# Kernel tuning notes

Hardware: AMD Instinct MI355X
Metric: run time of the kernel (lower is better)

## Reference

```python
import jax, jax.numpy as jnp
import numpy as np

D, N, F_IN, F_OUT = 2, 4096, 128, 128
DENSITY = 0.005  # avg degree ~20 per row in the 0/1 attention graphs
NEG_INF = -1e30


def setup_inputs() -> dict:
    key = jax.random.key(0)
    ks = jax.random.split(key, 12)
    X = jax.random.normal(ks[0], (D, N, F_IN), dtype=jnp.float32)
    # Dense Laplacian operator used in torch.sparse.mm(L[i], h_p); scaled so tanh stays non-degenerate
    L = jax.random.normal(ks[1], (D, N, N), dtype=jnp.float32) / np.float32(np.sqrt(N))
    # Upper/lower adjacency: 0/1 matrices (GATLayer extracts edges via adj == 1)
    L_u = (jax.random.uniform(ks[2], (D, N, N)) < DENSITY).astype(jnp.float32)
    L_d = (jax.random.uniform(ks[3], (D, N, N)) < DENSITY).astype(jnp.float32)
    s = np.float32(0.05)
    Wp = jax.random.normal(ks[4], (D, F_IN, F_OUT), dtype=jnp.float32) * s
    Ws = jax.random.normal(ks[5], (D, F_IN, F_OUT), dtype=jnp.float32) * s
    Wu = jax.random.normal(ks[6], (D, F_IN, F_OUT), dtype=jnp.float32) * s
    au1 = jax.random.normal(ks[7], (D, F_OUT), dtype=jnp.float32) * s
    au2 = jax.random.normal(ks[8], (D, F_OUT), dtype=jnp.float32) * s
    Wd = jax.random.normal(ks[9], (D, F_IN, F_OUT), dtype=jnp.float32) * s
    ad1 = jax.random.normal(ks[10], (D, F_OUT), dtype=jnp.float32) * s
    ad2 = jax.random.normal(ks[11], (D, F_OUT), dtype=jnp.float32) * s
    return {"X": X, "L": L, "L_u": L_u, "L_d": L_d,
            "Wp": Wp, "Ws": Ws, "Wu": Wu, "au1": au1, "au2": au2,
            "Wd": Wd, "ad1": ad1, "ad2": ad2, "dimensions": D}


def _gat(x, adj, W, a1, a2):
    # GATLayer.forward with boundary=False: linear -> edge scores -> LeakyReLU ->
    # row-wise softmax restricted to adj==1 entries -> sparse mm.
    h = x @ W                                   # [N, F_OUT]
    s1 = h @ a1                                 # [N]  (a_1 linear, bias=False)
    s2 = h @ a2                                 # [N]
    scores = jax.nn.leaky_relu(s1[:, None] + s2[None, :])  # [N, N], slope 0.01
    mask = adj == 1.0
    scores = jnp.where(mask, scores, NEG_INF)
    attn = jax.nn.softmax(scores, axis=1)
    attn = jnp.where(mask, attn, 0.0)           # zero rows with no edges (sparse softmax semantics)
    return attn @ h                             # [N, F_OUT]


def _san_dim(x, L, Lu, Ld, Wp, Ws, Wu, au1, au2, Wd, ad1, ad2):
    h_p = jnp.tanh(L @ (x @ Wp))
    h_s = jnp.tanh(x @ Ws)
    h_u = jnp.tanh(_gat(x, Lu, Wu, au1, au2))
    h_d = jnp.tanh(_gat(x, Ld, Wd, ad1, ad2))
    return h_s + h_u + h_d + h_p


def reference(X, L, L_u, L_d, Wp, Ws, Wu, au1, au2, Wd, ad1, ad2, dimensions):
    # vmap over the `dimensions` simplex levels (all per-level params stacked on axis 0)
    return jax.vmap(_san_dim)(X, L, L_u, L_d, Wp, Ws, Wu, au1, au2, Wd, ad1, ad2)
```

## Files before the change

### kernel.cpp

```cpp
#include <hip/hip_runtime.h>
#include <hip/hip_bf16.h>

#define NN 4096
#define FD 128
#define NDIM 2
#define CAP 256

typedef unsigned long long u64;

#define OFF_HMAT 0
#define OFF_SVEC 3145728
#define OFF_HP   3178496
#define OFF_GU   7372800
#define OFF_GD   8421376
#define OFF_H0T  9469952
#define OFF_MASK 9994240

typedef _Float16 f16x8 __attribute__((ext_vector_type(8)));
typedef float f32x4 __attribute__((ext_vector_type(4)));
typedef float f32x4v __attribute__((ext_vector_type(4)));
typedef unsigned long long u64x2 __attribute__((ext_vector_type(2)));

union P4 { _Float16 h[4]; int2 i2; };

__device__ __forceinline__ float f4get(const float4& v, int j) {
    return j == 0 ? v.x : j == 1 ? v.y : j == 2 ? v.z : v.w;
}

__global__ __launch_bounds__(256) void k_xw(
    const float* __restrict__ X, const float* __restrict__ Wp,
    const float* __restrict__ Wsm, const float* __restrict__ Wu,
    const float* __restrict__ Wd, float* __restrict__ hmat,
    _Float16* __restrict__ h0T) {
  int d = blockIdx.z, p = blockIdx.y;
  int r0 = blockIdx.x * 128;
  const float* W = (p == 0 ? Wp : p == 1 ? Wsm : p == 2 ? Wu : Wd) + (size_t)d * FD * FD;
  const float* Xd = X + ((size_t)d * NN + r0) * FD;
  __shared__ int4 As4[2048];
  __shared__ int4 Bs4[2048];
  char* As = (char*)As4; char* Bs = (char*)Bs4;
  int t = threadIdx.x;

#pragma unroll 4
  for (int u = 0; u < 16; u++) {
    int id = t + u * 256;
    int row = id >> 5, k4 = (id & 31) * 4;
    float4 v = *(const float4*)(Xd + (size_t)row * FD + k4);
    P4 pk;
    pk.h[0] = (_Float16)v.x; pk.h[1] = (_Float16)v.y;
    pk.h[2] = (_Float16)v.z; pk.h[3] = (_Float16)v.w;
    int off = (row * 256 + k4 * 2) ^ ((row & 7) << 4);
    *(int2*)(As + off) = pk.i2;
  }
#pragma unroll 4
  for (int u = 0; u < 16; u++) {
    int id = t + u * 256;
    int k = id >> 5, n4 = (id & 31) * 4;
    float4 v = *(const float4*)(W + (size_t)k * FD + n4);
#pragma unroll
    for (int j = 0; j < 4; j++) {
      int n = n4 + j;
      int off = (n * 256 + k * 2) ^ ((n & 7) << 4);
      *(_Float16*)(Bs + off) = (_Float16)f4get(v, j);
    }
  }
  __syncthreads();

  int w = t >> 6, l = t & 63;
  int lr = l & 15, lkb = (l >> 4) * 16;
  f32x4 acc[2][8] = {};
#pragma unroll
  for (int kb = 0; kb < 4; kb++) {
    f16x8 a[2], b[8];
#pragma unroll
    for (int m = 0; m < 2; m++) {
      int row = w * 32 + m * 16 + lr;
      int off = (row * 256 + kb * 64 + lkb) ^ ((row & 7) << 4);
      a[m] = *(const f16x8*)(As + off);
    }
#pragma unroll
    for (int n = 0; n < 8; n++) {
      int rn = n * 16 + lr;
      int off = (rn * 256 + kb * 64 + lkb) ^ ((rn & 7) << 4);
      b[n] = *(const f16x8*)(Bs + off);
    }
#pragma unroll
    for (int m = 0; m < 2; m++)
#pragma unroll
      for (int n = 0; n < 8; n++)
        acc[m][n] = __builtin_amdgcn_mfma_f32_16x16x32_f16(a[m], b[n], acc[m][n], 0, 0, 0);
  }

  if (p == 0) {
    _Float16* hT = h0T + (size_t)d * FD * NN;
#pragma unroll
    for (int m = 0; m < 2; m++)
#pragma unroll
      for (int n = 0; n < 8; n++) {
        int col = n * 16 + lr;
        int grow = r0 + w * 32 + m * 16 + (l >> 4) * 4;
        P4 pk;
#pragma unroll
        for (int r = 0; r < 4; r++) pk.h[r] = (_Float16)acc[m][n][r];
        *(int2*)(hT + (size_t)col * NN + grow) = pk.i2;
      }
  } else {
    float* o = hmat + ((size_t)(d * 3 + p - 1) * NN + r0) * FD;
#pragma unroll
    for (int m = 0; m < 2; m++)
#pragma unroll
      for (int n = 0; n < 8; n++)
#pragma unroll
        for (int r = 0; r < 4; r++)
          o[(size_t)(w * 32 + m * 16 + (l >> 4) * 4 + r) * FD + n * 16 + lr] = acc[m][n][r];
  }
}

__global__ __launch_bounds__(256) void k_svec(
    const float* __restrict__ hmat, const float* __restrict__ au1,
    const float* __restrict__ au2, const float* __restrict__ ad1,
    const float* __restrict__ ad2, float* __restrict__ svec) {
  int v = blockIdx.y, d = blockIdx.z;
  int w = threadIdx.x >> 6, lane = threadIdx.x & 63;
  int i = blockIdx.x * 4 + w;
  const float* a = (v == 0 ? au1 : v == 1 ? au2 : v == 2 ? ad1 : ad2) + (size_t)d * FD;
  const float* h = hmat + ((size_t)(d * 3 + 1 + (v >> 1)) * NN + i) * FD;
  float x = h[lane] * a[lane] + h[64 + lane] * a[64 + lane];
#pragma unroll
  for (int o = 1; o < 64; o <<= 1) x += __shfl_xor(x, o);
  if (lane == 0) svec[(size_t)(d * 4 + v) * NN + i] = x;
}

__global__ __launch_bounds__(256) void k_lgemm(
    const float* __restrict__ L, const _Float16* __restrict__ h0T,
    float* __restrict__ hp) {
  int d = blockIdx.z, ks = blockIdx.y;
  int r0 = blockIdx.x * 64;
  const float* Lr = L + (size_t)d * NN * NN;
  const _Float16* hT = h0T + (size_t)d * FD * NN;
  __shared__ int4 As4[512];
  __shared__ int4 Bs4[1024];
  char* As = (char*)As4; char* Bs = (char*)Bs4;
  int t = threadIdx.x;
  int w = t >> 6, l = t & 63;
  int lr = l & 15, lkb = (l >> 4) * 16;
  f32x4 acc[8] = {};
  int kbeg = ks * 1024;
  for (int kk = kbeg; kk < kbeg + 1024; kk += 64) {
#pragma unroll
    for (int u = 0; u < 4; u++) {
      int id = t + u * 256;
      int row = id >> 4, k4 = (id & 15) * 4;
      f32x4v v = __builtin_nontemporal_load(
          (const f32x4v*)(Lr + (size_t)(r0 + row) * NN + kk) + (k4 >> 2));
      P4 pk;
      pk.h[0] = (_Float16)v[0]; pk.h[1] = (_Float16)v[1];
      pk.h[2] = (_Float16)v[2]; pk.h[3] = (_Float16)v[3];
      int off = (row * 128 + k4 * 2) ^ ((row & 7) << 4);
      *(int2*)(As + off) = pk.i2;
    }
#pragma unroll
    for (int u = 0; u < 4; u++) {
      int id = t + u * 256;
      int n = id >> 3, k8 = (id & 7) * 8;
      int4 v = *(const int4*)(hT + (size_t)n * NN + kk + k8);
      int off = (n * 128 + k8 * 2) ^ ((n & 7) << 4);
      *(int4*)(Bs + off) = v;
    }
    __syncthreads();
#pragma unroll
    for (int kb = 0; kb < 2; kb++) {
      int row = w * 16 + lr;
      int offA = (row * 128 + kb * 64 + lkb) ^ ((row & 7) << 4);
      f16x8 a = *(const f16x8*)(As + offA);
      f16x8 b[8];
#pragma unroll
      for (int n = 0; n < 8; n++) {
        int rn = n * 16 + lr;
        int off = (rn * 128 + kb * 64 + lkb) ^ ((rn & 7) << 4);
        b[n] = *(const f16x8*)(Bs + off);
      }
#pragma unroll
      for (int n = 0; n < 8; n++)
        acc[n] = __builtin_amdgcn_mfma_f32_16x16x32_f16(a, b[n], acc[n], 0, 0, 0);
    }
    __syncthreads();
  }
  float* o = hp + ((size_t)(d * 4 + ks) * NN + r0) * FD;
#pragma unroll
  for (int n = 0; n < 8; n++)
#pragma unroll
    for (int r = 0; r < 4; r++)
      o[(size_t)(w * 16 + (l >> 4) * 4 + r) * FD + n * 16 + lr] = acc[n][r];
}

__global__ __launch_bounds__(256) void k_pack(
    const float* __restrict__ Lu, const float* __restrict__ Ldn,
    u64* __restrict__ mask) {
  int lane = threadIdx.x & 63;
  int wid = (blockIdx.x * 256 + threadIdx.x) >> 6;
  int nw = (gridDim.x * 256) >> 6;
  const int QTOT = 4 * NN * 2;
  for (int quad = wid; quad < QTOT; quad += nw) {
    int p = quad >> 13;
    int rq = quad & 8191;
    int row = rq >> 1, half = rq & 1;
    const float* src = ((p & 1) ? Ldn : Lu) +
                       ((size_t)(p >> 1) * NN + row) * (size_t)NN + half * 2048;
    f32x4v v[8];
#pragma unroll
    for (int q = 0; q < 4; q++) {
      const f32x4v* s4 = (const f32x4v*)(src + q * 512);
      v[2 * q]     = __builtin_nontemporal_load(s4 + lane);
      v[2 * q + 1] = __builtin_nontemporal_load(s4 + 64 + lane);
    }
    u64* o = mask + ((size_t)p * NN + row) * 64 + half * 32;
#pragma unroll
    for (int q = 0; q < 4; q++) {
      u64 m0 = __ballot(v[2 * q][0] == 1.0f);
      u64 m1 = __ballot(v[2 * q][1] == 1.0f);
      u64 m2 = __ballot(v[2 * q][2] == 1.0f);
      u64 m3 = __ballot(v[2 * q][3] == 1.0f);
      u64 m4 = __ballot(v[2 * q + 1][0] == 1.0f);
      u64 m5 = __ballot(v[2 * q + 1][1] == 1.0f);
      u64 m6 = __ballot(v[2 * q + 1][2] == 1.0f);
      u64 m7 = __ballot(v[2 * q + 1][3] == 1.0f);
      if (lane == 0) {
        u64x2 a0 = {m0, m1}, a1 = {m2, m3}, a2 = {m4, m5}, a3 = {m6, m7};
        __builtin_nontemporal_store(a0, (u64x2*)(o + q * 8 + 0));
        __builtin_nontemporal_store(a1, (u64x2*)(o + q * 8 + 2));
        __builtin_nontemporal_store(a2, (u64x2*)(o + q * 8 + 4));
        __builtin_nontemporal_store(a3, (u64x2*)(o + q * 8 + 6));
      }
    }
  }
}

__global__ __launch_bounds__(256) void k_gat2(
    const u64* __restrict__ mask, const float* __restrict__ hmat,
    const float* __restrict__ svec, float* __restrict__ gu,
    float* __restrict__ gd) {
  int d = blockIdx.z, a = blockIdx.y;
  int w = threadIdx.x >> 6, lane = threadIdx.x & 63;
  int i = blockIdx.x * 4 + w;
  const u64* mrow = mask + ((size_t)((d * 2 + a) * NN) + i) * 64;
  const float* h = hmat + (size_t)(d * 3 + 1 + a) * NN * FD;
  const float* s1 = svec + (size_t)(d * 4 + 2 * a) * NN;
  const float* s2 = svec + (size_t)(d * 4 + 2 * a + 1) * NN;
  float* g = (a ? gd : gu) + ((size_t)d * NN + i) * FD;

  __shared__ int ej[4][CAP];
  __shared__ float wt[4][CAP];

  u64 m = mrow[lane];
  int c = __popcll(m);
  int pre = c;
#pragma unroll
  for (int o = 1; o < 64; o <<= 1) {
    int tv = __shfl_up(pre, o);
    if (lane >= o) pre += tv;
  }
  int cnt = __shfl(pre, 63);
  int base = pre - c;
  int colbase = (lane >> 2) * 256 + (lane & 3);
  while (m) {
    int b = __ffsll((unsigned long long)m) - 1;
    m &= m - 1;
    if (base < CAP) ej[w][base] = colbase + b * 4;
    base++;
  }
  cnt = min(cnt, CAP);

  float s1i = s1[i];
  float mx = -1e30f;
  for (int e0 = 0; e0 < cnt; e0 += 64) {
    int e = e0 + lane;
    float sc = -1e30f;
    if (e < cnt) {
      int j = ej[w][e];
      float x = s1i + s2[j];
      sc = x > 0.0f ? x : 0.01f * x;
      wt[w][e] = sc;
    }
    mx = fmaxf(mx, sc);
  }
#pragma unroll
  for (int o = 1; o < 64; o <<= 1) mx = fmaxf(mx, __shfl_xor(mx, o));
  float sum = 0.0f;
  for (int e0 = 0; e0 < cnt; e0 += 64) {
    int e = e0 + lane;
    float pv = 0.0f;
    if (e < cnt) {
      pv = expf(wt[w][e] - mx);
      wt[w][e] = pv;
    }
    sum += pv;
  }
#pragma unroll
  for (int o = 1; o < 64; o <<= 1) sum += __shfl_xor(sum, o);
  float inv = (cnt > 0) ? 1.0f / sum : 0.0f;

  float acc0 = 0.0f, acc1 = 0.0f;
  int e = 0;
  for (; e + 4 <= cnt; e += 4) {
    const float* r0 = h + (size_t)ej[w][e + 0] * FD;
    const float* r1 = h + (size_t)ej[w][e + 1] * FD;
    const float* r2 = h + (size_t)ej[w][e + 2] * FD;
    const float* r3 = h + (size_t)ej[w][e + 3] * FD;
    float w0 = wt[w][e + 0] * inv, w1 = wt[w][e + 1] * inv;
    float w2 = wt[w][e + 2] * inv, w3 = wt[w][e + 3] * inv;
    float a0 = r0[lane], b0 = r0[64 + lane];
    float a1 = r1[lane], b1 = r1[64 + lane];
    float a2 = r2[lane], b2 = r2[64 + lane];
    float a3 = r3[lane], b3 = r3[64 + lane];
    acc0 += w0 * a0 + w1 * a1 + w2 * a2 + w3 * a3;
    acc1 += w0 * b0 + w1 * b1 + w2 * b2 + w3 * b3;
  }
  for (; e < cnt; e++) {
    float wg = wt[w][e] * inv;
    const float* hr = h + (size_t)ej[w][e] * FD;
    acc0 += wg * hr[lane];
    acc1 += wg * hr[64 + lane];
  }
  g[lane] = acc0;
  g[64 + lane] = acc1;
}

__global__ __launch_bounds__(256) void k_combine(
    const float* __restrict__ hmat, const float* __restrict__ hp,
    const float* __restrict__ gu, const float* __restrict__ gd,
    float* __restrict__ out) {
  const size_t tot4 = (size_t)NDIM * NN * FD / 4;
  for (size_t i4 = (size_t)blockIdx.x * blockDim.x + threadIdx.x; i4 < tot4;
       i4 += (size_t)gridDim.x * blockDim.x) {
    size_t i = i4 * 4;
    int d = (int)(i >> 19);
    size_t rem = i & 524287;
    float4 hs = *(const float4*)(hmat + ((size_t)(d * 3) << 19) + rem);
    float4 p0 = *(const float4*)(hp + ((size_t)(d * 4 + 0) << 19) + rem);
    float4 p1 = *(const float4*)(hp + ((size_t)(d * 4 + 1) << 19) + rem);
    float4 p2 = *(const float4*)(hp + ((size_t)(d * 4 + 2) << 19) + rem);
    float4 p3 = *(const float4*)(hp + ((size_t)(d * 4 + 3) << 19) + rem);
    float4 u = *(const float4*)(gu + ((size_t)d << 19) + rem);
    float4 dd = *(const float4*)(gd + ((size_t)d << 19) + rem);
    float4 o;
    o.x = tanhf(hs.x) + tanhf(u.x) + tanhf(dd.x) + tanhf(p0.x + p1.x + p2.x + p3.x);
    o.y = tanhf(hs.y) + tanhf(u.y) + tanhf(dd.y) + tanhf(p0.y + p1.y + p2.y + p3.y);
    o.z = tanhf(hs.z) + tanhf(u.z) + tanhf(dd.z) + tanhf(p0.z + p1.z + p2.z + p3.z);
    o.w = tanhf(hs.w) + tanhf(u.w) + tanhf(dd.w) + tanhf(p0.w + p1.w + p2.w + p3.w);
    *(float4*)(out + i) = o;
  }
}

extern "C" void kernel_launch(void* const* d_in, const int* in_sizes, int n_in,
                              void* d_out, int out_size, void* d_ws, size_t ws_size,
                              hipStream_t stream) {
  const float* X   = (const float*)d_in[0];
  const float* L   = (const float*)d_in[1];
  const float* Lu  = (const float*)d_in[2];
  const float* Ldn = (const float*)d_in[3];
  const float* Wp  = (const float*)d_in[4];
  const float* Wsm = (const float*)d_in[5];
  const float* Wu  = (const float*)d_in[6];
  const float* au1 = (const float*)d_in[7];
  const float* au2 = (const float*)d_in[8];
  const float* Wd  = (const float*)d_in[9];
  const float* ad1 = (const float*)d_in[10];
  const float* ad2 = (const float*)d_in[11];
  float* out = (float*)d_out;
  float* ws = (float*)d_ws;

  float* hmat = ws + OFF_HMAT;
  float* svec = ws + OFF_SVEC;
  float* hp   = ws + OFF_HP;
  float* gu   = ws + OFF_GU;
  float* gd   = ws + OFF_GD;
  _Float16* h0T = (_Float16*)(ws + OFF_H0T);
  u64* mask = (u64*)(ws + OFF_MASK);

  k_xw<<<dim3(NN / 128, 4, NDIM), 256, 0, stream>>>(X, Wp, Wsm, Wu, Wd, hmat, h0T);
  k_svec<<<dim3(NN / 4, 4, NDIM), 256, 0, stream>>>(hmat, au1, au2, ad1, ad2, svec);
  k_pack<<<2048, 256, 0, stream>>>(Lu, Ldn, mask);
  k_lgemm<<<dim3(NN / 64, 4, NDIM), 256, 0, stream>>>(L, h0T, hp);
  k_gat2<<<dim3(NN / 4, 2, NDIM), 256, 0, stream>>>(mask, hmat, svec, gu, gd);
  k_combine<<<1024, 256, 0, stream>>>(hmat, hp, gu, gd, out);
}
```

Baseline: 133.5 us.

## Merge L-GEMM with mask packing, fuse GAT with final combine

Runs the dense L GEMM and the adjacency bit-packing in one launch, using disjoint block ranges, so the compute-heavy and bandwidth-heavy work can share the GPU at the same time. The two GAT aggregations are fused with the tanh combine into one kernel, which removes the gu/gd intermediate buffers and their extra read/write pass. The fused GAT kernel uses twice the shared memory per block, which may reduce occupancy. It also does both attention passes serially within each wave.

```diff
diff --git a/kernel.cpp b/kernel.cpp
--- a/kernel.cpp
+++ b/kernel.cpp
@@ -11,10 +11,8 @@
 #define OFF_HMAT 0
 #define OFF_SVEC 3145728
 #define OFF_HP   3178496
-#define OFF_GU   7372800
-#define OFF_GD   8421376
-#define OFF_H0T  9469952
-#define OFF_MASK 9994240
+#define OFF_H0T  7372800
+#define OFF_MASK 7897088
 
 typedef _Float16 f16x8 __attribute__((ext_vector_type(8)));
 typedef float f32x4 __attribute__((ext_vector_type(4)));
@@ -131,224 +129,211 @@
   if (lane == 0) svec[(size_t)(d * 4 + v) * NN + i] = x;
 }
 
-__global__ __launch_bounds__(256) void k_lgemm(
+__global__ __launch_bounds__(256) void k_mega(
     const float* __restrict__ L, const _Float16* __restrict__ h0T,
-    float* __restrict__ hp) {
-  int d = blockIdx.z, ks = blockIdx.y;
-  int r0 = blockIdx.x * 64;
-  const float* Lr = L + (size_t)d * NN * NN;
-  const _Float16* hT = h0T + (size_t)d * FD * NN;
-  __shared__ int4 As4[512];
-  __shared__ int4 Bs4[1024];
-  char* As = (char*)As4; char* Bs = (char*)Bs4;
-  int t = threadIdx.x;
-  int w = t >> 6, l = t & 63;
-  int lr = l & 15, lkb = (l >> 4) * 16;
-  f32x4 acc[8] = {};
-  int kbeg = ks * 1024;
-  for (int kk = kbeg; kk < kbeg + 1024; kk += 64) {
-#pragma unroll
-    for (int u = 0; u < 4; u++) {
-      int id = t + u * 256;
-      int row = id >> 4, k4 = (id & 15) * 4;
-      f32x4v v = __builtin_nontemporal_load(
-          (const f32x4v*)(Lr + (size_t)(r0 + row) * NN + kk) + (k4 >> 2));
-      P4 pk;
-      pk.h[0] = (_Float16)v[0]; pk.h[1] = (_Float16)v[1];
-      pk.h[2] = (_Float16)v[2]; pk.h[3] = (_Float16)v[3];
-      int off = (row * 128 + k4 * 2) ^ ((row & 7) << 4);
-      *(int2*)(As + off) = pk.i2;
-    }
-#pragma unroll
-    for (int u = 0; u < 4; u++) {
-      int id = t + u * 256;
-      int n = id >> 3, k8 = (id & 7) * 8;
-      int4 v = *(const int4*)(hT + (size_t)n * NN + kk + k8);
-      int off = (n * 128 + k8 * 2) ^ ((n & 7) << 4);
-      *(int4*)(Bs + off) = v;
-    }
-    __syncthreads();
-#pragma unroll
-    for (int kb = 0; kb < 2; kb++) {
-      int row = w * 16 + lr;
-      int offA = (row * 128 + kb * 64 + lkb) ^ ((row & 7) << 4);
-      f16x8 a = *(const f16x8*)(As + offA);
-      f16x8 b[8];
-#pragma unroll
-      for (int n = 0; n < 8; n++) {
-        int rn = n * 16 + lr;
-        int off = (rn * 128 + kb * 64 + lkb) ^ ((rn & 7) << 4);
-        b[n] = *(const f16x8*)(Bs + off);
-      }
-#pragma unroll
-      for (int n = 0; n < 8; n++)
-        acc[n] = __builtin_amdgcn_mfma_f32_16x16x32_f16(a, b[n], acc[n], 0, 0, 0);
-    }
-    __syncthreads();
-  }
-  float* o = hp + ((size_t)(d * 4 + ks) * NN + r0) * FD;
-#pragma unroll
-  for (int n = 0; n < 8; n++)
-#pragma unroll
-    for (int r = 0; r < 4; r++)
-      o[(size_t)(w * 16 + (l >> 4) * 4 + r) * FD + n * 16 + lr] = acc[n][r];
-}
-
-__global__ __launch_bounds__(256) void k_pack(
+    float* __restrict__ hp,
     const float* __restrict__ Lu, const float* __restrict__ Ldn,
     u64* __restrict__ mask) {
-  int lane = threadIdx.x & 63;
-  int wid = (blockIdx.x * 256 + threadIdx.x) >> 6;
-  int nw = (gridDim.x * 256) >> 6;
-  const int QTOT = 4 * NN * 2;
-  for (int quad = wid; quad < QTOT; quad += nw) {
-    int p = quad >> 13;
-    int rq = quad & 8191;
-    int row = rq >> 1, half = rq & 1;
-    const float* src = ((p & 1) ? Ldn : Lu) +
-                       ((size_t)(p >> 1) * NN + row) * (size_t)NN + half * 2048;
-    f32x4v v[8];
-#pragma unroll
-    for (int q = 0; q < 4; q++) {
-      const f32x4v* s4 = (const f32x4v*)(src + q * 512);
-      v[2 * q]     = __builtin_nontemporal_load(s4 + lane);
-      v[2 * q + 1] = __builtin_nontemporal_load(s4 + 64 + lane);
-    }
-    u64* o = mask + ((size_t)p * NN + row) * 64 + half * 32;
-#pragma unroll
-    for (int q = 0; q < 4; q++) {
-      u64 m0 = __ballot(v[2 * q][0] == 1.0f);
-      u64 m1 = __ballot(v[2 * q][1] == 1.0f);
-      u64 m2 = __ballot(v[2 * q][2] == 1.0f);
-      u64 m3 = __ballot(v[2 * q][3] == 1.0f);
-      u64 m4 = __ballot(v[2 * q + 1][0] == 1.0f);
-      u64 m5 = __ballot(v[2 * q + 1][1] == 1.0f);
-      u64 m6 = __ballot(v[2 * q + 1][2] == 1.0f);
-      u64 m7 = __ballot(v[2 * q + 1][3] == 1.0f);
-      if (lane == 0) {
-        u64x2 a0 = {m0, m1}, a1 = {m2, m3}, a2 = {m4, m5}, a3 = {m6, m7};
-        __builtin_nontemporal_store(a0, (u64x2*)(o + q * 8 + 0));
-        __builtin_nontemporal_store(a1, (u64x2*)(o + q * 8 + 2));
-        __builtin_nontemporal_store(a2, (u64x2*)(o + q * 8 + 4));
-        __builtin_nontemporal_store(a3, (u64x2*)(o + q * 8 + 6));
-      }
-    }
-  }
-}
-
-__global__ __launch_bounds__(256) void k_gat2(
+  __shared__ int4 sm4[1536];
+  int t = threadIdx.x, w = t >> 6, lane = t & 63;
+
+  if (blockIdx.x < 512) {
+    int b = blockIdx.x;
+    int r0 = (b & 63) * 64, ks = (b >> 6) & 3, d = b >> 8;
+    const float* Lr = L + (size_t)d * NN * NN;
+    const _Float16* hT = h0T + (size_t)d * FD * NN;
+    char* As = (char*)sm4;
+    char* Bs = (char*)(sm4 + 512);
+    int lr = lane & 15, lkb = (lane >> 4) * 16;
+    f32x4 acc[8] = {};
+    int kbeg = ks * 1024;
+    for (int kk = kbeg; kk < kbeg + 1024; kk += 64) {
+#pragma unroll
+      for (int u = 0; u < 4; u++) {
+        int id = t + u * 256;
+        int row = id >> 4, k4 = (id & 15) * 4;
+        f32x4v v = __builtin_nontemporal_load(
+            (const f32x4v*)(Lr + (size_t)(r0 + row) * NN + kk) + (k4 >> 2));
+        P4 pk;
+        pk.h[0] = (_Float16)v[0]; pk.h[1] = (_Float16)v[1];
+        pk.h[2] = (_Float16)v[2]; pk.h[3] = (_Float16)v[3];
+        int off = (row * 128 + k4 * 2) ^ ((row & 7) << 4);
+        *(int2*)(As + off) = pk.i2;
+      }
+#pragma unroll
+      for (int u = 0; u < 4; u++) {
+        int id = t + u * 256;
+        int n = id >> 3, k8 = (id & 7) * 8;
+        int4 v = *(const int4*)(hT + (size_t)n * NN + kk + k8);
+        int off = (n * 128 + k8 * 2) ^ ((n & 7) << 4);
+        *(int4*)(Bs + off) = v;
+      }
+      __syncthreads();
+#pragma unroll
+      for (int kb = 0; kb < 2; kb++) {
+        int row = w * 16 + lr;
+        int offA = (row * 128 + kb * 64 + lkb) ^ ((row & 7) << 4);
+        f16x8 a = *(const f16x8*)(As + offA);
+        f16x8 bb[8];
+#pragma unroll
+        for (int n = 0; n < 8; n++) {
+          int rn = n * 16 + lr;
+          int off = (rn * 128 + kb * 64 + lkb) ^ ((rn & 7) << 4);
+          bb[n] = *(const f16x8*)(Bs + off);
+        }
+#pragma unroll
+        for (int n = 0; n < 8; n++)
+          acc[n] = __builtin_amdgcn_mfma_f32_16x16x32_f16(a, bb[n], acc[n], 0, 0, 0);
+      }
+      __syncthreads();
+    }
+    float* o = hp + ((size_t)(d * 4 + ks) * NN + r0) * FD;
+#pragma unroll
+    for (int n = 0; n < 8; n++)
+#pragma unroll
+      for (int r = 0; r < 4; r++)
+        o[(size_t)(w * 16 + (lane >> 4) * 4 + r) * FD + n * 16 + lr] = acc[n][r];
+    return;
+  }
+
+  int hr = (blockIdx.x - 512) * 4 + w;
+  int p = hr >> 13;
+  int rq = hr & 8191;
+  int row = rq >> 1, half = rq & 1;
+  const float* src = ((p & 1) ? Ldn : Lu) +
+                     ((size_t)(p >> 1) * NN + row) * (size_t)NN + half * 2048;
+  f32x4v v[8];
+#pragma unroll
+  for (int q = 0; q < 4; q++) {
+    const f32x4v* s4 = (const f32x4v*)(src + q * 512);
+    v[2 * q]     = __builtin_nontemporal_load(s4 + lane);
+    v[2 * q + 1] = __builtin_nontemporal_load(s4 + 64 + lane);
+  }
+  u64* o = mask + ((size_t)p * NN + row) * 64 + half * 32;
+#pragma unroll
+  for (int q = 0; q < 4; q++) {
+    u64 m0 = __ballot(v[2 * q][0] == 1.0f);
+    u64 m1 = __ballot(v[2 * q][1] == 1.0f);
+    u64 m2 = __ballot(v[2 * q][2] == 1.0f);
+    u64 m3 = __ballot(v[2 * q][3] == 1.0f);
+    u64 m4 = __ballot(v[2 * q + 1][0] == 1.0f);
+    u64 m5 = __ballot(v[2 * q + 1][1] == 1.0f);
+    u64 m6 = __ballot(v[2 * q + 1][2] == 1.0f);
+    u64 m7 = __ballot(v[2 * q + 1][3] == 1.0f);
+    if (lane == 0) {
+      u64x2 a0 = {m0, m1}, a1 = {m2, m3}, a2 = {m4, m5}, a3 = {m6, m7};
+      __builtin_nontemporal_store(a0, (u64x2*)(o + q * 8 + 0));
+      __builtin_nontemporal_store(a1, (u64x2*)(o + q * 8 + 2));
+      __builtin_nontemporal_store(a2, (u64x2*)(o + q * 8 + 4));
+      __builtin_nontemporal_store(a3, (u64x2*)(o + q * 8 + 6));
+    }
+  }
+}
+
+__global__ __launch_bounds__(256) void k_gatc(
     const u64* __restrict__ mask, const float* __restrict__ hmat,
-    const float* __restrict__ svec, float* __restrict__ gu,
-    float* __restrict__ gd) {
-  int d = blockIdx.z, a = blockIdx.y;
+    const float* __restrict__ svec, const float* __restrict__ hp,
+    float* __restrict__ out) {
+  int d = blockIdx.y;
   int w = threadIdx.x >> 6, lane = threadIdx.x & 63;
   int i = blockIdx.x * 4 + w;
-  const u64* mrow = mask + ((size_t)((d * 2 + a) * NN) + i) * 64;
-  const float* h = hmat + (size_t)(d * 3 + 1 + a) * NN * FD;
-  const float* s1 = svec + (size_t)(d * 4 + 2 * a) * NN;
-  const float* s2 = svec + (size_t)(d * 4 + 2 * a + 1) * NN;
-  float* g = (a ? gd : gu) + ((size_t)d * NN + i) * FD;
-
-  __shared__ int ej[4][CAP];
-  __shared__ float wt[4][CAP];
-
-  u64 m = mrow[lane];
-  int c = __popcll(m);
-  int pre = c;
-#pragma unroll
-  for (int o = 1; o < 64; o <<= 1) {
-    int tv = __shfl_up(pre, o);
-    if (lane >= o) pre += tv;
-  }
-  int cnt = __shfl(pre, 63);
-  int base = pre - c;
-  int colbase = (lane >> 2) * 256 + (lane & 3);
-  while (m) {
-    int b = __ffsll((unsigned long long)m) - 1;
-    m &= m - 1;
-    if (base < CAP) ej[w][base] = colbase + b * 4;
-    base++;
-  }
-  cnt = min(cnt, CAP);
-
-  float s1i = s1[i];
-  float mx = -1e30f;
-  for (int e0 = 0; e0 < cnt; e0 += 64) {
-    int e = e0 + lane;
-    float sc = -1e30f;
-    if (e < cnt) {
-      int j = ej[w][e];
-      float x = s1i + s2[j];
-      sc = x > 0.0f ? x : 0.01f * x;
-      wt[w][e] = sc;
-    }
-    mx = fmaxf(mx, sc);
-  }
-#pragma unroll
-  for (int o = 1; o < 64; o <<= 1) mx = fmaxf(mx, __shfl_xor(mx, o));
-  float sum = 0.0f;
-  for (int e0 = 0; e0 < cnt; e0 += 64) {
-    int e = e0 + lane;
-    float pv = 0.0f;
-    if (e < cnt) {
-      pv = expf(wt[w][e] - mx);
-      wt[w][e] = pv;
-    }
-    sum += pv;
-  }
-#pragma unroll
-  for (int o = 1; o < 64; o <<= 1) sum += __shfl_xor(sum, o);
-  float inv = (cnt > 0) ? 1.0f / sum : 0.0f;
-
-  float acc0 = 0.0f, acc1 = 0.0f;
-  int e = 0;
-  for (; e + 4 <= cnt; e += 4) {
-    const float* r0 = h + (size_t)ej[w][e + 0] * FD;
-    const float* r1 = h + (size_t)ej[w][e + 1] * FD;
-    const float* r2 = h + (size_t)ej[w][e + 2] * FD;
-    const float* r3 = h + (size_t)ej[w][e + 3] * FD;
-    float w0 = wt[w][e + 0] * inv, w1 = wt[w][e + 1] * inv;
-    float w2 = wt[w][e + 2] * inv, w3 = wt[w][e + 3] * inv;
-    float a0 = r0[lane], b0 = r0[64 + lane];
-    float a1 = r1[lane], b1 = r1[64 + lane];
-    float a2 = r2[lane], b2 = r2[64 + lane];
-    float a3 = r3[lane], b3 = r3[64 + lane];
-    acc0 += w0 * a0 + w1 * a1 + w2 * a2 + w3 * a3;
-    acc1 += w0 * b0 + w1 * b1 + w2 * b2 + w3 * b3;
-  }
-  for (; e < cnt; e++) {
-    float wg = wt[w][e] * inv;
-    const float* hr = h + (size_t)ej[w][e] * FD;
-    acc0 += wg * hr[lane];
-    acc1 += wg * hr[64 + lane];
-  }
-  g[lane] = acc0;
-  g[64 + lane] = acc1;
-}
-
-__global__ __launch_bounds__(256) void k_combine(
-    const float* __restrict__ hmat, const float* __restrict__ hp,
-    const float* __restrict__ gu, const float* __restrict__ gd,
-    float* __restrict__ out) {
-  const size_t tot4 = (size_t)NDIM * NN * FD / 4;
-  for (size_t i4 = (size_t)blockIdx.x * blockDim.x + threadIdx.x; i4 < tot4;
-       i4 += (size_t)gridDim.x * blockDim.x) {
-    size_t i = i4 * 4;
-    int d = (int)(i >> 19);
-    size_t rem = i & 524287;
-    float4 hs = *(const float4*)(hmat + ((size_t)(d * 3) << 19) + rem);
-    float4 p0 = *(const float4*)(hp + ((size_t)(d * 4 + 0) << 19) + rem);
-    float4 p1 = *(const float4*)(hp + ((size_t)(d * 4 + 1) << 19) + rem);
-    float4 p2 = *(const float4*)(hp + ((size_t)(d * 4 + 2) << 19) + rem);
-    float4 p3 = *(const float4*)(hp + ((size_t)(d * 4 + 3) << 19) + rem);
-    float4 u = *(const float4*)(gu + ((size_t)d << 19) + rem);
-    float4 dd = *(const float4*)(gd + ((size_t)d << 19) + rem);
-    float4 o;
-    o.x = tanhf(hs.x) + tanhf(u.x) + tanhf(dd.x) + tanhf(p0.x + p1.x + p2.x + p3.x);
-    o.y = tanhf(hs.y) + tanhf(u.y) + tanhf(dd.y) + tanhf(p0.y + p1.y + p2.y + p3.y);
-    o.z = tanhf(hs.z) + tanhf(u.z) + tanhf(dd.z) + tanhf(p0.z + p1.z + p2.z + p3.z);
-    o.w = tanhf(hs.w) + tanhf(u.w) + tanhf(dd.w) + tanhf(p0.w + p1.w + p2.w + p3.w);
-    *(float4*)(out + i) = o;
+
+  __shared__ int ej[4][2][CAP];
+  __shared__ float wt[4][2][CAP];
+
+  float ga[2][2];
+#pragma unroll
+  for (int a = 0; a < 2; a++) {
+    const u64* mrow = mask + ((size_t)((d * 2 + a) * NN) + i) * 64;
+    const float* h = hmat + (size_t)(d * 3 + 1 + a) * NN * FD;
+    const float* s1 = svec + (size_t)(d * 4 + 2 * a) * NN;
+    const float* s2 = svec + (size_t)(d * 4 + 2 * a + 1) * NN;
+
+    u64 m = mrow[lane];
+    int c = __popcll(m);
+    int pre = c;
+#pragma unroll
+    for (int o = 1; o < 64; o <<= 1) {
+      int tv = __shfl_up(pre, o);
+      if (lane >= o) pre += tv;
+    }
+    int cnt = __shfl(pre, 63);
+    int base = pre - c;
+    int colbase = (lane >> 2) * 256 + (lane & 3);
+    while (m) {
+      int b = __ffsll((unsigned long long)m) - 1;
+      m &= m - 1;
+      if (base < CAP) ej[w][a][base] = colbase + b * 4;
+      base++;
+    }
+    cnt = min(cnt, CAP);
+
+    float s1i = s1[i];
+    float mx = -1e30f;
+    for (int e0 = 0; e0 < cnt; e0 += 64) {
+      int e = e0 + lane;
+      float sc = -1e30f;
+      if (e < cnt) {
+        int j = ej[w][a][e];
+        float x = s1i + s2[j];
+        sc = x > 0.0f ? x : 0.01f * x;
+        wt[w][a][e] = sc;
+      }
+      mx = fmaxf(mx, sc);
+    }
+#pragma unroll
+    for (int o = 1; o < 64; o <<= 1) mx = fmaxf(mx, __shfl_xor(mx, o));
+    float sum = 0.0f;
+    for (int e0 = 0; e0 < cnt; e0 += 64) {
+      int e = e0 + lane;
+      float pv = 0.0f;
+      if (e < cnt) {
+        pv = expf(wt[w][a][e] - mx);
+        wt[w][a][e] = pv;
+      }
+      sum += pv;
+    }
+#pragma unroll
+    for (int o = 1; o < 64; o <<= 1) sum += __shfl_xor(sum, o);
+    float inv = (cnt > 0) ? 1.0f / sum : 0.0f;
+
+    float acc0 = 0.0f, acc1 = 0.0f;
+    int e = 0;
+    for (; e + 4 <= cnt; e += 4) {
+      const float* r0 = h + (size_t)ej[w][a][e + 0] * FD;
+      const float* r1 = h + (size_t)ej[w][a][e + 1] * FD;
+      const float* r2 = h + (size_t)ej[w][a][e + 2] * FD;
+      const float* r3 = h + (size_t)ej[w][a][e + 3] * FD;
+      float w0 = wt[w][a][e + 0] * inv, w1 = wt[w][a][e + 1] * inv;
+      float w2 = wt[w][a][e + 2] * inv, w3 = wt[w][a][e + 3] * inv;
+      float a0 = r0[lane], b0 = r0[64 + lane];
+      float a1 = r1[lane], b1 = r1[64 + lane];
+      float a2 = r2[lane], b2 = r2[64 + lane];
+      float a3 = r3[lane], b3 = r3[64 + lane];
+      acc0 += w0 * a0 + w1 * a1 + w2 * a2 + w3 * a3;
+      acc1 += w0 * b0 + w1 * b1 + w2 * b2 + w3 * b3;
+    }
+    for (; e < cnt; e++) {
+      float wg = wt[w][a][e] * inv;
+      const float* hr = h + (size_t)ej[w][a][e] * FD;
+      acc0 += wg * hr[lane];
+      acc1 += wg * hr[64 + lane];
+    }
+    ga[a][0] = acc0;
+    ga[a][1] = acc1;
+  }
+
+  const float* hs = hmat + ((size_t)(d * 3) * NN + i) * FD;
+  const float* h0 = hp + ((size_t)(d * 4 + 0) * NN + i) * FD;
+  const float* h1 = hp + ((size_t)(d * 4 + 1) * NN + i) * FD;
+  const float* h2 = hp + ((size_t)(d * 4 + 2) * NN + i) * FD;
+  const float* h3 = hp + ((size_t)(d * 4 + 3) * NN + i) * FD;
+  float* o = out + ((size_t)d * NN + i) * FD;
+#pragma unroll
+  for (int hf = 0; hf < 2; hf++) {
+    int col = hf * 64 + lane;
+    float ps = h0[col] + h1[col] + h2[col] + h3[col];
+    o[col] = tanhf(hs[col]) + tanhf(ga[0][hf]) + tanhf(ga[1][hf]) + tanhf(ps);
   }
 }
 
@@ -373,15 +358,11 @@
   float* hmat = ws + OFF_HMAT;
   float* svec = ws + OFF_SVEC;
   float* hp   = ws + OFF_HP;
-  float* gu   = ws + OFF_GU;
-  float* gd   = ws + OFF_GD;
   _Float16* h0T = (_Float16*)(ws + OFF_H0T);
   u64* mask = (u64*)(ws + OFF_MASK);
 
   k_xw<<<dim3(NN / 128, 4, NDIM), 256, 0, stream>>>(X, Wp, Wsm, Wu, Wd, hmat, h0T);
   k_svec<<<dim3(NN / 4, 4, NDIM), 256, 0, stream>>>(hmat, au1, au2, ad1, ad2, svec);
-  k_pack<<<2048, 256, 0, stream>>>(Lu, Ldn, mask);
-  k_lgemm<<<dim3(NN / 64, 4, NDIM), 256, 0, stream>>>(L, h0T, hp);
-  k_gat2<<<dim3(NN / 4, 2, NDIM), 256, 0, stream>>>(mask, hmat, svec, gu, gd);
-  k_combine<<<1024, 256, 0, stream>>>(hmat, hp, gu, gd, out);
-}
+  k_mega<<<dim3(512 + 8192, 1, 1), 256, 0, stream>>>(L, h0T, hp, Lu, Ldn, mask);
+  k_gatc<<<dim3(NN / 4, NDIM, 1), 256, 0, stream>>>(mask, hmat, svec, hp, out);
+}
```

Result: faster. 124.5 us (-6.7%).
